# Kernel optimization log

Measured on AMD Instinct MI355X. Metric: run time of the kernel, lower is better.

Reference implementation:

```python
import jax, jax.numpy as jnp
import numpy as np

TEMPERATURE = 1.0

def _rope_cos_sin(T, D):
    # inv_freq over even indices 0..D step 2 -> D//2 freqs
    inv_freq = 1.0 / (10000.0 ** (jnp.arange(0, D, 2, dtype=jnp.float32) / D))
    t = jnp.arange(T, dtype=jnp.float32)
    freqs = jnp.einsum('i,j->ij', t, inv_freq)          # [T, D//2]
    emb = jnp.concatenate([freqs, freqs], axis=-1)      # [T, D]
    return jnp.cos(emb), jnp.sin(emb)                   # each [T, D]

def _apply_rope(x, cos, sin):
    # x: [B,H,T,D]; cos/sin: [T,D] broadcast over B,H
    D = x.shape[-1]
    half = D // 2
    x1, x2 = x[..., :half], x[..., half:2 * half]
    c = cos[None, None, :, :half]
    s = sin[None, None, :, :half]
    rot = jnp.concatenate([x1 * c - x2 * s, x1 * s + x2 * c], axis=-1)
    if D > 2 * half:
        rot = jnp.concatenate([rot, x[..., 2 * half:]], axis=-1)
    return rot

def setup_inputs() -> dict:
    key = jax.random.key(0)
    kq, kk, kv = jax.random.split(key, 3)
    B, H, T, D = 2, 16, 2048, 64
    return {
        'q': jax.random.normal(kq, (B, H, T, D), dtype=jnp.float32),
        'k': jax.random.normal(kk, (B, H, T, D), dtype=jnp.float32),
        'v': jax.random.normal(kv, (B, H, T, D), dtype=jnp.float32),
    }

def reference(q, k, v):
    B, H, T, D = q.shape
    cos, sin = _rope_cos_sin(T, D)
    qr = _apply_rope(q, cos, sin)
    kr = _apply_rope(k, cos, sin)
    scale = jnp.sqrt(jnp.float32(D)) * TEMPERATURE
    scores = jnp.einsum('bhtd,bhsd->bhts', qr, kr) / scale  # [B,H,T,T]
    # original subtracts row max then softmax; identical to stable softmax
    attn = jax.nn.softmax(scores, axis=-1)
    out = jnp.einsum('bhts,bhsd->bhtd', attn, v)
    return out, attn
```

## Files before the change

kernel.cpp:

```cpp
#include <hip/hip_runtime.h>
#include <hip/hip_bf16.h>
#include <math.h>


#define T_SEQ  2048
#define D_HEAD 64
#define BH_N   32
#define NCH    32
#define OUT_ELEMS (BH_N * T_SEQ * D_HEAD)

typedef __attribute__((ext_vector_type(8))) short bf16x8;
typedef __attribute__((ext_vector_type(4))) float f32x4;

__device__ __forceinline__ unsigned short f2bf(float x) {
    __hip_bfloat16 h = __float2bfloat16(x);
    return *reinterpret_cast<unsigned short*>(&h);
}

__device__ __forceinline__ int swz(int o) { return o ^ (((o >> 7) & 7) << 4); }
__device__ __forceinline__ int tswz(int row, int bcol) {
    return row * 256 + (bcol ^ ((row & 7) << 4));
}

__global__ void rope_table_kernel(float* __restrict__ ctab, float* __restrict__ stab) {
    int i = blockIdx.x * blockDim.x + threadIdx.x;
    if (i >= T_SEQ * 32) return;
    int t = i >> 5;
    int j = i & 31;
    float invf = powf(10000.0f, -(float)j / 32.0f);
    float a = (float)t * invf;
    ctab[i] = cosf(a);
    stab[i] = sinf(a);
}

__global__ __launch_bounds__(256)
void ropebf16_kernel(const float* __restrict__ Q, const float* __restrict__ K,
                     const float* __restrict__ ctab, const float* __restrict__ stab,
                     unsigned short* __restrict__ Qb, unsigned short* __restrict__ Kb,
                     float qscale)
{
    const int r  = blockIdx.x * 16 + (threadIdx.x >> 4);
    const int c4 = threadIdx.x & 15;
    const int t  = r & (T_SEQ - 1);
    const float* X = blockIdx.y ? K : Q;
    unsigned short* H = blockIdx.y ? Kb : Qb;
    const float scale = blockIdx.y ? 1.0f : qscale;
    const float4* xr = (const float4*)(X + (size_t)r * 64);
    float4 a = xr[c4];
    float4 b = xr[c4 ^ 8];
    float4 c = ((const float4*)(ctab + t * 32))[c4 & 7];
    float4 s = ((const float4*)(stab + t * 32))[c4 & 7];
    float4 ro;
    if (c4 < 8) {
        ro.x = a.x * c.x - b.x * s.x; ro.y = a.y * c.y - b.y * s.y;
        ro.z = a.z * c.z - b.z * s.z; ro.w = a.w * c.w - b.w * s.w;
    } else {
        ro.x = a.x * c.x + b.x * s.x; ro.y = a.y * c.y + b.y * s.y;
        ro.z = a.z * c.z + b.z * s.z; ro.w = a.w * c.w + b.w * s.w;
    }
    ushort4 h;
    h.x = f2bf(ro.x * scale); h.y = f2bf(ro.y * scale);
    h.z = f2bf(ro.z * scale); h.w = f2bf(ro.w * scale);
    *(ushort4*)(H + (size_t)r * 64 + c4 * 4) = h;
}

__global__ __launch_bounds__(256)
void vtbf16_kernel(const float* __restrict__ V, unsigned short* __restrict__ Vt)
{
    __shared__ float tile[64][65];
    const int bh = blockIdx.y;
    const int tt = blockIdx.x;
    const float* vg = V + ((size_t)bh * T_SEQ + tt * 64) * 64;
    #pragma unroll
    for (int i = 0; i < 4; ++i) {
        const int row = (threadIdx.x >> 4) + i * 16;
        const int c4  = threadIdx.x & 15;
        float4 a = *(const float4*)(vg + (size_t)row * 64 + c4 * 4);
        tile[row][c4 * 4 + 0] = a.x; tile[row][c4 * 4 + 1] = a.y;
        tile[row][c4 * 4 + 2] = a.z; tile[row][c4 * 4 + 3] = a.w;
    }
    __syncthreads();
    #pragma unroll
    for (int i = 0; i < 4; ++i) {
        const int d   = (threadIdx.x >> 4) + i * 16;
        const int tc4 = threadIdx.x & 15;
        ushort4 h;
        h.x = f2bf(tile[tc4 * 4 + 0][d]);
        h.y = f2bf(tile[tc4 * 4 + 1][d]);
        h.z = f2bf(tile[tc4 * 4 + 2][d]);
        h.w = f2bf(tile[tc4 * 4 + 3][d]);
        *(unsigned short*)&h;
        *(ushort4*)(Vt + ((size_t)bh * 64 + d) * T_SEQ + tt * 64 + tc4 * 4) = h;
    }
}

__global__ __launch_bounds__(256, 4)
void attn_mfma_kernel(const unsigned short* __restrict__ Qb,
                      const unsigned short* __restrict__ Kb,
                      const unsigned short* __restrict__ Vt,
                      float* __restrict__ out, float* __restrict__ attn)
{
    __shared__ __align__(16) unsigned short kbuf[3][64][64];
    __shared__ __align__(16) float tbuf[4][16 * 64];

    const int tid  = threadIdx.x;
    const int lane = tid & 63;
    const int w    = tid >> 6;
    const int lrow = lane & 15;
    const int lgrp = lane >> 4;

    const int lid = blockIdx.x;
    const int vid = (lid & 7) * 128 + (lid >> 3);
    const int bh  = vid >> 5;
    const int m   = vid & 31;
    const int t0  = m * 64 + w * 16;

    const size_t base = (size_t)bh * T_SEQ * D_HEAD;
    const char* kgb = (const char*)(Kb + base);
    const unsigned short* kgs = Kb + base;
    const unsigned short* vgb = Vt + (size_t)bh * 64 * T_SEQ;

    {
        bf16x8 qa[4][2];
        #pragma unroll
        for (int rg = 0; rg < 4; ++rg) {
            const unsigned short* qp = Qb + base + (size_t)(m * 64 + rg * 16 + lrow) * 64 + lgrp * 8;
            qa[rg][0] = *(const bf16x8*)(qp);
            qa[rg][1] = *(const bf16x8*)(qp + 32);
        }
        float rpa[4] = {0.f, 0.f, 0.f, 0.f};
        for (int c = 0; c < 8; ++c) {
            const int cc = w * 8 + c;
            bf16x8 kf[4][2];
            #pragma unroll
            for (int nt = 0; nt < 4; ++nt) {
                const unsigned short* kp = kgs + (size_t)(cc * 64 + nt * 16 + lrow) * 64 + lgrp * 8;
                kf[nt][0] = *(const bf16x8*)(kp);
                kf[nt][1] = *(const bf16x8*)(kp + 32);
            }
            #pragma unroll
            for (int rg = 0; rg < 4; ++rg) {
                float r0 = 0.f;
                #pragma unroll
                for (int nt = 0; nt < 4; ++nt) {
                    f32x4 acc = (f32x4){0.f, 0.f, 0.f, 0.f};
                    acc = __builtin_amdgcn_mfma_f32_16x16x32_bf16(kf[nt][0], qa[rg][0], acc, 0, 0, 0);
                    acc = __builtin_amdgcn_mfma_f32_16x16x32_bf16(kf[nt][1], qa[rg][1], acc, 0, 0, 0);
                    r0 += __builtin_amdgcn_exp2f(acc[0]) + __builtin_amdgcn_exp2f(acc[1])
                        + __builtin_amdgcn_exp2f(acc[2]) + __builtin_amdgcn_exp2f(acc[3]);
                }
                rpa[rg] += r0;
            }
        }
        #pragma unroll
        for (int rg = 0; rg < 4; ++rg) {
            rpa[rg] += __shfl_xor(rpa[rg], 16, 64);
            rpa[rg] += __shfl_xor(rpa[rg], 32, 64);
        }
        if (lane < 16) {
            #pragma unroll
            for (int rg = 0; rg < 4; ++rg)
                tbuf[0][w * 64 + rg * 16 + lrow] = rpa[rg];
        }
    }
    __builtin_amdgcn_sched_barrier(0);
    __builtin_amdgcn_s_barrier();
    const float inv = 1.0f / (tbuf[0][0 * 64 + w * 16 + lrow] + tbuf[0][1 * 64 + w * 16 + lrow]
                            + tbuf[0][2 * 64 + w * 16 + lrow] + tbuf[0][3 * 64 + w * 16 + lrow]);
    __builtin_amdgcn_sched_barrier(0);
    __builtin_amdgcn_s_barrier();

    const int so0 = w * 1024 + lane * 16;
    const int so1 = so0 + 4096;
    const int sq0 = swz(so0);
    const int sq1 = swz(so1);
    char* klds = (char*)&kbuf[0][0][0];
    char* tlds = (char*)&tbuf[w][0];

#define STAGE_K(b, cc) do { \
    __builtin_amdgcn_global_load_lds((const unsigned int*)(kgb + (size_t)(cc) * 8192 + sq0), \
        (unsigned int*)(klds + (b) * 8192 + w * 1024), 16, 0, 0); \
    __builtin_amdgcn_global_load_lds((const unsigned int*)(kgb + (size_t)(cc) * 8192 + sq1), \
        (unsigned int*)(klds + (b) * 8192 + 4096 + w * 1024), 16, 0, 0); \
} while (0)

    bf16x8 qf0, qf1;
    {
        const unsigned short* qp = Qb + base + (size_t)(t0 + lrow) * 64 + lgrp * 8;
        qf0 = *(const bf16x8*)(qp);
        qf1 = *(const bf16x8*)(qp + 32);
    }

    f32x4 o4[4];
    #pragma unroll
    for (int nd = 0; nd < 4; ++nd) o4[nd] = (f32x4){0.f, 0.f, 0.f, 0.f};

    float* abase = attn + (size_t)bh * T_SEQ * T_SEQ;

    STAGE_K(0, 0);
    STAGE_K(1, 1);
    bf16x8 vf[8];
    #pragma unroll
    for (int nd = 0; nd < 4; ++nd)
        #pragma unroll
        for (int ks = 0; ks < 2; ++ks)
            vf[nd * 2 + ks] = *(const bf16x8*)(vgb + (size_t)(nd * 16 + lrow) * T_SEQ
                                               + ks * 32 + lgrp * 8);
    asm volatile("s_waitcnt vmcnt(10)" ::: "memory");

    for (int cc = 0; cc < NCH; ++cc) {
        __builtin_amdgcn_s_barrier();
        __builtin_amdgcn_sched_barrier(0);

        const char* kb = klds + (cc % 3) * 8192;
        f32x4 s4[4];
        #pragma unroll
        for (int nt = 0; nt < 4; ++nt) {
            const int o = (nt * 16 + lrow) * 128 + lgrp * 16;
            bf16x8 a0 = *(const bf16x8*)(kb + swz(o));
            bf16x8 a1 = *(const bf16x8*)(kb + swz(o + 64));
            f32x4 acc = (f32x4){0.f, 0.f, 0.f, 0.f};
            acc = __builtin_amdgcn_mfma_f32_16x16x32_bf16(a0, qf0, acc, 0, 0, 0);
            acc = __builtin_amdgcn_mfma_f32_16x16x32_bf16(a1, qf1, acc, 0, 0, 0);
            s4[nt] = acc;
        }
        #pragma unroll
        for (int nt = 0; nt < 4; ++nt) {
            s4[nt][0] = __builtin_amdgcn_exp2f(s4[nt][0]) * inv;
            s4[nt][1] = __builtin_amdgcn_exp2f(s4[nt][1]) * inv;
            s4[nt][2] = __builtin_amdgcn_exp2f(s4[nt][2]) * inv;
            s4[nt][3] = __builtin_amdgcn_exp2f(s4[nt][3]) * inv;
        }
        #pragma unroll
        for (int nt = 0; nt < 4; ++nt)
            *(f32x4*)(tlds + tswz(lrow, (nt * 16 + lgrp * 4) * 4)) = s4[nt];
        asm volatile("s_waitcnt lgkmcnt(0)" ::: "memory");
        __builtin_amdgcn_sched_barrier(0);

        #pragma unroll
        for (int ks = 0; ks < 2; ++ks) {
            f32x4 pa0 = *(const f32x4*)(tlds + tswz(lrow, (ks * 32 + lgrp * 8) * 4));
            f32x4 pa1 = *(const f32x4*)(tlds + tswz(lrow, (ks * 32 + lgrp * 8 + 4) * 4));
            bf16x8 pa;
            pa[0] = (short)f2bf(pa0[0]); pa[1] = (short)f2bf(pa0[1]);
            pa[2] = (short)f2bf(pa0[2]); pa[3] = (short)f2bf(pa0[3]);
            pa[4] = (short)f2bf(pa1[0]); pa[5] = (short)f2bf(pa1[1]);
            pa[6] = (short)f2bf(pa1[2]); pa[7] = (short)f2bf(pa1[3]);
            #pragma unroll
            for (int nd = 0; nd < 4; ++nd)
                o4[nd] = __builtin_amdgcn_mfma_f32_16x16x32_bf16(pa, vf[nd * 2 + ks], o4[nd], 0, 0, 0);
        }
        f32x4 tr[4];
        #pragma unroll
        for (int i = 0; i < 4; ++i)
            tr[i] = *(const f32x4*)(tlds + tswz(i * 4 + (lane >> 4), (lane & 15) * 16));
        __builtin_amdgcn_sched_barrier(0);
        if (cc + 1 < NCH) {
            #pragma unroll
            for (int nd = 0; nd < 4; ++nd)
                #pragma unroll
                for (int ks = 0; ks < 2; ++ks)
                    vf[nd * 2 + ks] = *(const bf16x8*)(vgb + (size_t)(nd * 16 + lrow) * T_SEQ
                                                       + (cc + 1) * 64 + ks * 32 + lgrp * 8);
        }
        if (cc + 2 < NCH) STAGE_K((cc + 2) % 3, cc + 2);
        __builtin_amdgcn_sched_barrier(0);
        #pragma unroll
        for (int i = 0; i < 4; ++i)
            __builtin_nontemporal_store(tr[i],
                (f32x4*)(abase + (size_t)(t0 + i * 4 + (lane >> 4)) * T_SEQ
                         + cc * 64 + (lane & 15) * 4));
        __builtin_amdgcn_sched_barrier(0);
        if (cc < NCH - 2)      { asm volatile("s_waitcnt vmcnt(18)" ::: "memory"); }
        else if (cc < NCH - 1) { asm volatile("s_waitcnt vmcnt(16)" ::: "memory"); }
    }

    #pragma unroll
    for (int nd = 0; nd < 4; ++nd)
        #pragma unroll
        for (int j = 0; j < 4; ++j)
            __builtin_nontemporal_store(o4[nd][j],
                out + base + (size_t)(t0 + lgrp * 4 + j) * D_HEAD + nd * 16 + lrow);

#undef STAGE_K
}

extern "C" void kernel_launch(void* const* d_in, const int* in_sizes, int n_in,
                              void* d_out, int out_size, void* d_ws, size_t ws_size,
                              hipStream_t stream) {
    const float* q = (const float*)d_in[0];
    const float* k = (const float*)d_in[1];
    const float* v = (const float*)d_in[2];
    float* out  = (float*)d_out;
    float* attn = out + (size_t)OUT_ELEMS;

    float* ctab = (float*)d_ws;
    float* stab = ctab + T_SEQ * 32;
    unsigned short* wsu = (unsigned short*)(stab + T_SEQ * 32);
    const size_t NE = (size_t)BH_N * T_SEQ * D_HEAD;
    unsigned short* Qb = wsu + 0 * NE;
    unsigned short* Kb = wsu + 1 * NE;
    unsigned short* Vt = wsu + 2 * NE;

    const float QSCALE = 0.18033688011112042f;

    rope_table_kernel<<<dim3((T_SEQ * 32 + 255) / 256), dim3(256), 0, stream>>>(ctab, stab);
    ropebf16_kernel<<<dim3(BH_N * T_SEQ / 16, 2), dim3(256), 0, stream>>>(q, k, ctab, stab, Qb, Kb, QSCALE);
    vtbf16_kernel<<<dim3(T_SEQ / 64, BH_N), dim3(256), 0, stream>>>(v, Vt);
    attn_mfma_kernel<<<dim3(BH_N * T_SEQ / 64), dim3(256), 0, stream>>>(Qb, Kb, Vt, out, attn);
}
```

Baseline: 196.4 us.

## Merge RoPE and V-transpose kernels; restructure row-sum pass and prefetch K earlier

```diff
diff --git a/kernel.cpp b/kernel.cpp
--- a/kernel.cpp
+++ b/kernel.cpp
@@ -34,63 +34,62 @@
 }
 
 __global__ __launch_bounds__(256)
-void ropebf16_kernel(const float* __restrict__ Q, const float* __restrict__ K,
-                     const float* __restrict__ ctab, const float* __restrict__ stab,
-                     unsigned short* __restrict__ Qb, unsigned short* __restrict__ Kb,
-                     float qscale)
-{
-    const int r  = blockIdx.x * 16 + (threadIdx.x >> 4);
-    const int c4 = threadIdx.x & 15;
-    const int t  = r & (T_SEQ - 1);
-    const float* X = blockIdx.y ? K : Q;
-    unsigned short* H = blockIdx.y ? Kb : Qb;
-    const float scale = blockIdx.y ? 1.0f : qscale;
-    const float4* xr = (const float4*)(X + (size_t)r * 64);
-    float4 a = xr[c4];
-    float4 b = xr[c4 ^ 8];
-    float4 c = ((const float4*)(ctab + t * 32))[c4 & 7];
-    float4 s = ((const float4*)(stab + t * 32))[c4 & 7];
-    float4 ro;
-    if (c4 < 8) {
-        ro.x = a.x * c.x - b.x * s.x; ro.y = a.y * c.y - b.y * s.y;
-        ro.z = a.z * c.z - b.z * s.z; ro.w = a.w * c.w - b.w * s.w;
-    } else {
-        ro.x = a.x * c.x + b.x * s.x; ro.y = a.y * c.y + b.y * s.y;
-        ro.z = a.z * c.z + b.z * s.z; ro.w = a.w * c.w + b.w * s.w;
-    }
-    ushort4 h;
-    h.x = f2bf(ro.x * scale); h.y = f2bf(ro.y * scale);
-    h.z = f2bf(ro.z * scale); h.w = f2bf(ro.w * scale);
-    *(ushort4*)(H + (size_t)r * 64 + c4 * 4) = h;
-}
-
-__global__ __launch_bounds__(256)
-void vtbf16_kernel(const float* __restrict__ V, unsigned short* __restrict__ Vt)
+void pre_kernel(const float* __restrict__ Q, const float* __restrict__ K,
+                const float* __restrict__ V,
+                const float* __restrict__ ctab, const float* __restrict__ stab,
+                unsigned short* __restrict__ Qb, unsigned short* __restrict__ Kb,
+                unsigned short* __restrict__ Vt, float qscale)
 {
     __shared__ float tile[64][65];
-    const int bh = blockIdx.y;
-    const int tt = blockIdx.x;
-    const float* vg = V + ((size_t)bh * T_SEQ + tt * 64) * 64;
-    #pragma unroll
-    for (int i = 0; i < 4; ++i) {
-        const int row = (threadIdx.x >> 4) + i * 16;
-        const int c4  = threadIdx.x & 15;
-        float4 a = *(const float4*)(vg + (size_t)row * 64 + c4 * 4);
-        tile[row][c4 * 4 + 0] = a.x; tile[row][c4 * 4 + 1] = a.y;
-        tile[row][c4 * 4 + 2] = a.z; tile[row][c4 * 4 + 3] = a.w;
-    }
-    __syncthreads();
-    #pragma unroll
-    for (int i = 0; i < 4; ++i) {
-        const int d   = (threadIdx.x >> 4) + i * 16;
-        const int tc4 = threadIdx.x & 15;
+    if (blockIdx.y < 2) {
+        const int r  = blockIdx.x * 16 + (threadIdx.x >> 4);
+        const int c4 = threadIdx.x & 15;
+        const int t  = r & (T_SEQ - 1);
+        const float* X = blockIdx.y ? K : Q;
+        unsigned short* H = blockIdx.y ? Kb : Qb;
+        const float scale = blockIdx.y ? 1.0f : qscale;
+        const float4* xr = (const float4*)(X + (size_t)r * 64);
+        float4 a = xr[c4];
+        float4 b = xr[c4 ^ 8];
+        float4 c = ((const float4*)(ctab + t * 32))[c4 & 7];
+        float4 s = ((const float4*)(stab + t * 32))[c4 & 7];
+        float4 ro;
+        if (c4 < 8) {
+            ro.x = a.x * c.x - b.x * s.x; ro.y = a.y * c.y - b.y * s.y;
+            ro.z = a.z * c.z - b.z * s.z; ro.w = a.w * c.w - b.w * s.w;
+        } else {
+            ro.x = a.x * c.x + b.x * s.x; ro.y = a.y * c.y + b.y * s.y;
+            ro.z = a.z * c.z + b.z * s.z; ro.w = a.w * c.w + b.w * s.w;
+        }
         ushort4 h;
-        h.x = f2bf(tile[tc4 * 4 + 0][d]);
-        h.y = f2bf(tile[tc4 * 4 + 1][d]);
-        h.z = f2bf(tile[tc4 * 4 + 2][d]);
-        h.w = f2bf(tile[tc4 * 4 + 3][d]);
-        *(unsigned short*)&h;
-        *(ushort4*)(Vt + ((size_t)bh * 64 + d) * T_SEQ + tt * 64 + tc4 * 4) = h;
+        h.x = f2bf(ro.x * scale); h.y = f2bf(ro.y * scale);
+        h.z = f2bf(ro.z * scale); h.w = f2bf(ro.w * scale);
+        *(ushort4*)(H + (size_t)r * 64 + c4 * 4) = h;
+    } else {
+        if (blockIdx.x >= 1024) return;
+        const int bh = blockIdx.x >> 5;
+        const int tt = blockIdx.x & 31;
+        const float* vg = V + ((size_t)bh * T_SEQ + tt * 64) * 64;
+        #pragma unroll
+        for (int i = 0; i < 4; ++i) {
+            const int row = (threadIdx.x >> 4) + i * 16;
+            const int c4  = threadIdx.x & 15;
+            float4 a = *(const float4*)(vg + (size_t)row * 64 + c4 * 4);
+            tile[row][c4 * 4 + 0] = a.x; tile[row][c4 * 4 + 1] = a.y;
+            tile[row][c4 * 4 + 2] = a.z; tile[row][c4 * 4 + 3] = a.w;
+        }
+        __syncthreads();
+        #pragma unroll
+        for (int i = 0; i < 4; ++i) {
+            const int d   = (threadIdx.x >> 4) + i * 16;
+            const int tc4 = threadIdx.x & 15;
+            ushort4 h;
+            h.x = f2bf(tile[tc4 * 4 + 0][d]);
+            h.y = f2bf(tile[tc4 * 4 + 1][d]);
+            h.z = f2bf(tile[tc4 * 4 + 2][d]);
+            h.w = f2bf(tile[tc4 * 4 + 3][d]);
+            *(ushort4*)(Vt + ((size_t)bh * 64 + d) * T_SEQ + tt * 64 + tc4 * 4) = h;
+        }
     }
 }
 
@@ -120,17 +119,38 @@
     const unsigned short* kgs = Kb + base;
     const unsigned short* vgb = Vt + (size_t)bh * 64 * T_SEQ;
 
+    const int so0 = w * 1024 + lane * 16;
+    const int so1 = so0 + 4096;
+    const int sq0 = swz(so0);
+    const int sq1 = swz(so1);
+    char* klds = (char*)&kbuf[0][0][0];
+    char* tlds = (char*)&tbuf[w][0];
+    float* psum = (float*)(klds + 16384);
+
+#define STAGE_K(b, cc) do { \
+    __builtin_amdgcn_global_load_lds((const unsigned int*)(kgb + (size_t)(cc) * 8192 + sq0), \
+        (unsigned int*)(klds + (b) * 8192 + w * 1024), 16, 0, 0); \
+    __builtin_amdgcn_global_load_lds((const unsigned int*)(kgb + (size_t)(cc) * 8192 + sq1), \
+        (unsigned int*)(klds + (b) * 8192 + 4096 + w * 1024), 16, 0, 0); \
+} while (0)
+
+    STAGE_K(0, 0);
+    STAGE_K(1, 1);
+
     {
-        bf16x8 qa[4][2];
-        #pragma unroll
-        for (int rg = 0; rg < 4; ++rg) {
-            const unsigned short* qp = Qb + base + (size_t)(m * 64 + rg * 16 + lrow) * 64 + lgrp * 8;
+        const int ch = w >> 1;
+        const int r2 = w & 1;
+        bf16x8 qa[2][2];
+        #pragma unroll
+        for (int rg = 0; rg < 2; ++rg) {
+            const unsigned short* qp = Qb + base
+                + (size_t)(m * 64 + r2 * 32 + rg * 16 + lrow) * 64 + lgrp * 8;
             qa[rg][0] = *(const bf16x8*)(qp);
             qa[rg][1] = *(const bf16x8*)(qp + 32);
         }
-        float rpa[4] = {0.f, 0.f, 0.f, 0.f};
-        for (int c = 0; c < 8; ++c) {
-            const int cc = w * 8 + c;
+        float rp00 = 0.f, rp01 = 0.f, rp10 = 0.f, rp11 = 0.f;
+        for (int c = 0; c < 16; ++c) {
+            const int cc = ch * 16 + c;
             bf16x8 kf[4][2];
             #pragma unroll
             for (int nt = 0; nt < 4; ++nt) {
@@ -139,50 +159,35 @@
                 kf[nt][1] = *(const bf16x8*)(kp + 32);
             }
             #pragma unroll
-            for (int rg = 0; rg < 4; ++rg) {
-                float r0 = 0.f;
+            for (int rg = 0; rg < 2; ++rg) {
                 #pragma unroll
                 for (int nt = 0; nt < 4; ++nt) {
                     f32x4 acc = (f32x4){0.f, 0.f, 0.f, 0.f};
                     acc = __builtin_amdgcn_mfma_f32_16x16x32_bf16(kf[nt][0], qa[rg][0], acc, 0, 0, 0);
                     acc = __builtin_amdgcn_mfma_f32_16x16x32_bf16(kf[nt][1], qa[rg][1], acc, 0, 0, 0);
-                    r0 += __builtin_amdgcn_exp2f(acc[0]) + __builtin_amdgcn_exp2f(acc[1])
-                        + __builtin_amdgcn_exp2f(acc[2]) + __builtin_amdgcn_exp2f(acc[3]);
+                    const float e = __builtin_amdgcn_exp2f(acc[0]) + __builtin_amdgcn_exp2f(acc[1])
+                                  + __builtin_amdgcn_exp2f(acc[2]) + __builtin_amdgcn_exp2f(acc[3]);
+                    if (rg == 0) { if (nt & 1) rp01 += e; else rp00 += e; }
+                    else         { if (nt & 1) rp11 += e; else rp10 += e; }
                 }
-                rpa[rg] += r0;
             }
         }
-        #pragma unroll
-        for (int rg = 0; rg < 4; ++rg) {
-            rpa[rg] += __shfl_xor(rpa[rg], 16, 64);
-            rpa[rg] += __shfl_xor(rpa[rg], 32, 64);
-        }
+        float rpA = rp00 + rp01;
+        float rpB = rp10 + rp11;
+        rpA += __shfl_xor(rpA, 16, 64);
+        rpA += __shfl_xor(rpA, 32, 64);
+        rpB += __shfl_xor(rpB, 16, 64);
+        rpB += __shfl_xor(rpB, 32, 64);
         if (lane < 16) {
-            #pragma unroll
-            for (int rg = 0; rg < 4; ++rg)
-                tbuf[0][w * 64 + rg * 16 + lrow] = rpa[rg];
+            psum[ch * 64 + r2 * 32 + lrow]      = rpA;
+            psum[ch * 64 + r2 * 32 + 16 + lrow] = rpB;
         }
     }
     __builtin_amdgcn_sched_barrier(0);
     __builtin_amdgcn_s_barrier();
-    const float inv = 1.0f / (tbuf[0][0 * 64 + w * 16 + lrow] + tbuf[0][1 * 64 + w * 16 + lrow]
-                            + tbuf[0][2 * 64 + w * 16 + lrow] + tbuf[0][3 * 64 + w * 16 + lrow]);
+    const float inv = 1.0f / (psum[w * 16 + lrow] + psum[64 + w * 16 + lrow]);
     __builtin_amdgcn_sched_barrier(0);
     __builtin_amdgcn_s_barrier();
-
-    const int so0 = w * 1024 + lane * 16;
-    const int so1 = so0 + 4096;
-    const int sq0 = swz(so0);
-    const int sq1 = swz(so1);
-    char* klds = (char*)&kbuf[0][0][0];
-    char* tlds = (char*)&tbuf[w][0];
-
-#define STAGE_K(b, cc) do { \
-    __builtin_amdgcn_global_load_lds((const unsigned int*)(kgb + (size_t)(cc) * 8192 + sq0), \
-        (unsigned int*)(klds + (b) * 8192 + w * 1024), 16, 0, 0); \
-    __builtin_amdgcn_global_load_lds((const unsigned int*)(kgb + (size_t)(cc) * 8192 + sq1), \
-        (unsigned int*)(klds + (b) * 8192 + 4096 + w * 1024), 16, 0, 0); \
-} while (0)
 
     bf16x8 qf0, qf1;
     {
@@ -197,8 +202,6 @@
 
     float* abase = attn + (size_t)bh * T_SEQ * T_SEQ;
 
-    STAGE_K(0, 0);
-    STAGE_K(1, 1);
     bf16x8 vf[8];
     #pragma unroll
     for (int nd = 0; nd < 4; ++nd)
@@ -206,7 +209,7 @@
         for (int ks = 0; ks < 2; ++ks)
             vf[nd * 2 + ks] = *(const bf16x8*)(vgb + (size_t)(nd * 16 + lrow) * T_SEQ
                                                + ks * 32 + lgrp * 8);
-    asm volatile("s_waitcnt vmcnt(10)" ::: "memory");
+    asm volatile("s_waitcnt vmcnt(8)" ::: "memory");
 
     for (int cc = 0; cc < NCH; ++cc) {
         __builtin_amdgcn_s_barrier();
@@ -305,7 +308,6 @@
     const float QSCALE = 0.18033688011112042f;
 
     rope_table_kernel<<<dim3((T_SEQ * 32 + 255) / 256), dim3(256), 0, stream>>>(ctab, stab);
-    ropebf16_kernel<<<dim3(BH_N * T_SEQ / 16, 2), dim3(256), 0, stream>>>(q, k, ctab, stab, Qb, Kb, QSCALE);
-    vtbf16_kernel<<<dim3(T_SEQ / 64, BH_N), dim3(256), 0, stream>>>(v, Vt);
+    pre_kernel<<<dim3(BH_N * T_SEQ / 16, 3), dim3(256), 0, stream>>>(q, k, v, ctab, stab, Qb, Kb, Vt, QSCALE);
     attn_mfma_kernel<<<dim3(BH_N * T_SEQ / 64), dim3(256), 0, stream>>>(Qb, Kb, Vt, out, attn);
 }
```

Measured after the change: 221.4 us. 12.7% more time.
